# Performance work log

Measured on AMD Instinct MI355X. Metric: run time of the kernel, lower is better.

Reference implementation:

```python
import jax, jax.numpy as jnp
import numpy as np

T, H, I = 8192, 2048, 768  # tokens, hidden_size, intermediate_size

def setup_inputs() -> dict:
    key = jax.random.key(0)
    k1, k2, k3, k4 = jax.random.split(key, 4)
    x = jax.random.normal(k1, (T, H), dtype=jnp.float32)
    # torch nn.Linear weight layout: [out_features, in_features]
    gate_w = jax.random.normal(k2, (I, H), dtype=jnp.float32) * (1.0 / np.sqrt(H))
    up_w = jax.random.normal(k3, (I, H), dtype=jnp.float32) * (1.0 / np.sqrt(H))
    down_w = jax.random.normal(k4, (H, I), dtype=jnp.float32) * (1.0 / np.sqrt(I))
    return {"x": x, "gate_w": gate_w, "up_w": up_w, "down_w": down_w}

def reference(x, gate_w, up_w, down_w):
    # fused SwiGLU MLP: down( silu(x @ gate^T) * (x @ up^T) )
    gate = jnp.einsum('th,ih->ti', x, gate_w)   # [T, I]
    up = jnp.einsum('th,ih->ti', x, up_w)       # [T, I]
    h = jax.nn.silu(gate) * up                   # [T, I]
    out = jnp.einsum('ti,hi->th', h, down_w)     # [T, H]
    return out
```

## Files before the change

kernel.cpp:

```cpp
#include <hip/hip_runtime.h>
#include <hip/hip_bf16.h>
#include <stdint.h>

#define T_DIM 8192
#define H_DIM 2048
#define I_DIM 768

typedef __bf16 bf16_t;
typedef bf16_t bf16x8 __attribute__((ext_vector_type(8)));
typedef bf16_t bf16x4 __attribute__((ext_vector_type(4)));
typedef float  f32x4  __attribute__((ext_vector_type(4)));

__device__ __forceinline__ void async_load16(const void* g, void* s) {
    __builtin_amdgcn_global_load_lds(
        (const __attribute__((address_space(1))) void*)g,
        (__attribute__((address_space(3))) void*)s, 16, 0, 0);
}

__global__ __launch_bounds__(256) void cvt_kernel(
    const float* __restrict__ X, const float* __restrict__ G,
    const float* __restrict__ U, const float* __restrict__ D,
    bf16_t* __restrict__ Xb, bf16_t* __restrict__ Gb,
    bf16_t* __restrict__ Ub, bf16_t* __restrict__ Db)
{
    const size_t N8X = (size_t)T_DIM * H_DIM / 8;
    const size_t N8W = (size_t)I_DIM * H_DIM / 8;
    const size_t total = N8X + 3 * N8W;
    for (size_t i = (size_t)blockIdx.x * blockDim.x + threadIdx.x; i < total;
         i += (size_t)gridDim.x * blockDim.x) {
        const float* s; bf16_t* d; size_t j = i;
        if (j < N8X) { s = X; d = Xb; }
        else {
            j -= N8X;
            if (j < N8W) { s = G; d = Gb; }
            else { j -= N8W;
                if (j < N8W) { s = U; d = Ub; }
                else { j -= N8W; s = D; d = Db; } }
        }
        float4 v0 = ((const float4*)s)[2 * j];
        float4 v1 = ((const float4*)s)[2 * j + 1];
        bf16x8 o;
        o[0] = (bf16_t)v0.x; o[1] = (bf16_t)v0.y; o[2] = (bf16_t)v0.z; o[3] = (bf16_t)v0.w;
        o[4] = (bf16_t)v1.x; o[5] = (bf16_t)v1.y; o[6] = (bf16_t)v1.z; o[7] = (bf16_t)v1.w;
        ((bf16x8*)d)[j] = o;
    }
}


__global__ __launch_bounds__(256) void gateup_kernel(
    const bf16_t* __restrict__ X,
    const bf16_t* __restrict__ Wg,
    const bf16_t* __restrict__ Wu,
    bf16_t* __restrict__ Hbuf)
{
    __shared__ __align__(16) bf16_t sA[128 * 64];
    __shared__ __align__(16) bf16_t sG[64 * 64];
    __shared__ __align__(16) bf16_t sU[64 * 64];

    const int tid   = threadIdx.x;
    const int lane  = tid & 63;
    const int wave  = tid >> 6;
    const int waveM = wave >> 1;
    const int waveN = wave & 1;
    const int quad  = lane >> 4;
    const int lrow  = lane & 15;

    const int blockM = blockIdx.x;
    const int blockN = blockIdx.y;

    f32x4 accG[4][2], accU[4][2];
#pragma unroll
    for (int i = 0; i < 4; i++)
#pragma unroll
        for (int j = 0; j < 2; j++) { accG[i][j] = (f32x4)(0.f); accU[i][j] = (f32x4)(0.f); }

    const bf16_t* Ab = X  + (size_t)(blockM * 128) * H_DIM;
    const bf16_t* Gw = Wg + (size_t)(blockN * 64) * H_DIM;
    const bf16_t* Uw = Wu + (size_t)(blockN * 64) * H_DIM;

    int aRow[4], aCol[4];
#pragma unroll
    for (int i = 0; i < 4; i++) {
        int s = tid + 256 * i;
        aRow[i] = s >> 3;
        aCol[i] = ((s & 7) ^ ((s >> 3) & 7)) * 8;
    }
    int wRow[2], wCol[2];
#pragma unroll
    for (int i = 0; i < 2; i++) {
        int s = tid + 256 * i;
        wRow[i] = s >> 3;
        wCol[i] = ((s & 7) ^ ((s >> 3) & 7)) * 8;
    }

    int aOff[4], wOff[2];
#pragma unroll
    for (int mi = 0; mi < 4; mi++) {
        int r = waveM * 64 + mi * 16 + lrow;
        aOff[mi] = r * 64 + ((quad ^ (r & 7)) * 8);
    }
#pragma unroll
    for (int ni = 0; ni < 2; ni++) {
        int r = waveN * 32 + ni * 16 + lrow;
        wOff[ni] = r * 64 + ((quad ^ (r & 7)) * 8);
    }

    for (int k0 = 0; k0 < H_DIM; k0 += 64) {
#pragma unroll
        for (int i = 0; i < 4; i++)
            async_load16(Ab + (size_t)aRow[i] * H_DIM + k0 + aCol[i],
                         &sA[(tid + 256 * i) * 8]);
#pragma unroll
        for (int i = 0; i < 2; i++) {
            async_load16(Gw + (size_t)wRow[i] * H_DIM + k0 + wCol[i],
                         &sG[(tid + 256 * i) * 8]);
            async_load16(Uw + (size_t)wRow[i] * H_DIM + k0 + wCol[i],
                         &sU[(tid + 256 * i) * 8]);
        }
        __syncthreads();

#pragma unroll
        for (int kk = 0; kk < 2; kk++) {
            const int kx = kk * 32;
            bf16x8 aF[4], gF[2], uF[2];
#pragma unroll
            for (int mi = 0; mi < 4; mi++)
                aF[mi] = *(const bf16x8*)&sA[aOff[mi] ^ kx];
#pragma unroll
            for (int ni = 0; ni < 2; ni++) {
                gF[ni] = *(const bf16x8*)&sG[wOff[ni] ^ kx];
                uF[ni] = *(const bf16x8*)&sU[wOff[ni] ^ kx];
            }
#pragma unroll
            for (int mi = 0; mi < 4; mi++)
#pragma unroll
                for (int ni = 0; ni < 2; ni++) {
                    accG[mi][ni] = __builtin_amdgcn_mfma_f32_16x16x32_bf16(aF[mi], gF[ni], accG[mi][ni], 0, 0, 0);
                    accU[mi][ni] = __builtin_amdgcn_mfma_f32_16x16x32_bf16(aF[mi], uF[ni], accU[mi][ni], 0, 0, 0);
                }
        }
        __syncthreads();
    }

#pragma unroll
    for (int mi = 0; mi < 4; mi++) {
#pragma unroll
        for (int ni = 0; ni < 2; ni++) {
#pragma unroll
            for (int r = 0; r < 4; r++) {
                int row = blockM * 128 + waveM * 64 + mi * 16 + quad * 4 + r;
                int col = blockN * 64 + waveN * 32 + ni * 16 + lrow;
                float g = accG[mi][ni][r];
                float u = accU[mi][ni][r];
                float h = (g / (1.f + __expf(-g))) * u;
                Hbuf[(size_t)row * I_DIM + col] = (bf16_t)h;
            }
        }
    }
}

__global__ __launch_bounds__(256, 4) void down_kernel(
    const bf16_t* __restrict__ Hbuf,
    const bf16_t* __restrict__ Wd,
    float* __restrict__ Out)
{
    __shared__ __align__(16) bf16_t sA[128 * 64];
    __shared__ __align__(16) bf16_t sB[128 * 64];

    const int tid   = threadIdx.x;
    const int lane  = tid & 63;
    const int wave  = tid >> 6;
    const int waveM = wave >> 1;
    const int waveN = wave & 1;
    const int quad  = lane >> 4;
    const int lrow  = lane & 15;

    const int blockM = blockIdx.x;
    const int blockN = blockIdx.y;

    f32x4 acc[4][4];
#pragma unroll
    for (int i = 0; i < 4; i++)
#pragma unroll
        for (int j = 0; j < 4; j++) acc[i][j] = (f32x4)(0.f);

    const bf16_t* Ab = Hbuf + (size_t)(blockM * 128) * I_DIM;
    const bf16_t* Bb = Wd   + (size_t)(blockN * 128) * I_DIM;

    int gRow[4], gCol[4];
#pragma unroll
    for (int i = 0; i < 4; i++) {
        int s = tid + 256 * i;
        gRow[i] = s >> 3;
        gCol[i] = ((s & 7) ^ ((s >> 3) & 7)) * 8;
    }

    int aOff[4], bOff[4];
#pragma unroll
    for (int mi = 0; mi < 4; mi++) {
        int r = waveM * 64 + mi * 16 + lrow;
        aOff[mi] = r * 64 + ((quad ^ (r & 7)) * 8);
    }
#pragma unroll
    for (int ni = 0; ni < 4; ni++) {
        int r = waveN * 64 + ni * 16 + lrow;
        bOff[ni] = r * 64 + ((quad ^ (r & 7)) * 8);
    }

    for (int k0 = 0; k0 < I_DIM; k0 += 64) {
#pragma unroll
        for (int i = 0; i < 4; i++) {
            async_load16(Ab + (size_t)gRow[i] * I_DIM + k0 + gCol[i],
                         &sA[(tid + 256 * i) * 8]);
            async_load16(Bb + (size_t)gRow[i] * I_DIM + k0 + gCol[i],
                         &sB[(tid + 256 * i) * 8]);
        }
        __syncthreads();

#pragma unroll
        for (int kk = 0; kk < 2; kk++) {
            const int kx = kk * 32;
            bf16x8 aF[4], bF[4];
#pragma unroll
            for (int mi = 0; mi < 4; mi++)
                aF[mi] = *(const bf16x8*)&sA[aOff[mi] ^ kx];
#pragma unroll
            for (int ni = 0; ni < 4; ni++)
                bF[ni] = *(const bf16x8*)&sB[bOff[ni] ^ kx];
#pragma unroll
            for (int mi = 0; mi < 4; mi++)
#pragma unroll
                for (int ni = 0; ni < 4; ni++)
                    acc[mi][ni] = __builtin_amdgcn_mfma_f32_16x16x32_bf16(aF[mi], bF[ni], acc[mi][ni], 0, 0, 0);
        }
        __syncthreads();
    }

#pragma unroll
    for (int mi = 0; mi < 4; mi++) {
#pragma unroll
        for (int ni = 0; ni < 4; ni++) {
#pragma unroll
            for (int r = 0; r < 4; r++) {
                int row = blockM * 128 + waveM * 64 + mi * 16 + quad * 4 + r;
                int col = blockN * 128 + waveN * 64 + ni * 16 + lrow;
                Out[(size_t)row * H_DIM + col] = acc[mi][ni][r];
            }
        }
    }
}

extern "C" void kernel_launch(void* const* d_in, const int* in_sizes, int n_in,
                              void* d_out, int out_size, void* d_ws, size_t ws_size,
                              hipStream_t stream) {
    const float* x  = (const float*)d_in[0];
    const float* gw = (const float*)d_in[1];
    const float* uw = (const float*)d_in[2];
    const float* dw = (const float*)d_in[3];
    float* out = (float*)d_out;

    bf16_t* xb = (bf16_t*)d_ws;
    bf16_t* gb = xb + (size_t)T_DIM * H_DIM;
    bf16_t* ub = gb + (size_t)I_DIM * H_DIM;
    bf16_t* db = ub + (size_t)I_DIM * H_DIM;
    bf16_t* hb = db + (size_t)I_DIM * H_DIM;

    cvt_kernel<<<2048, 256, 0, stream>>>(x, gw, uw, dw, xb, gb, ub, db);
    gateup_kernel<<<dim3(T_DIM / 128, I_DIM / 64), 256, 0, stream>>>(xb, gb, ub, hb);
    down_kernel<<<dim3(T_DIM / 128, H_DIM / 128), 256, 0, stream>>>(hb, db, out);
}
```

Before: 238.4 us.

## Shrink gate/up K-tile to 32 and drop LDS swizzle

The gate/up GEMM now stages a K-slice of 32 instead of 64 per iteration, with unswizzled row-major LDS tiles, and loads fragments into registers before a second barrier so the MFMAs run outside the LDS critical section. LDS per block is halved, which could raise occupancy. The cost is twice as many loop iterations and barriers per K, and the plain layout with a 64-byte row stride may bring back LDS bank conflicts on fragment reads.

New measurement: 223.2 us. 1.07x faster.

```diff
diff --git a/kernel.cpp b/kernel.cpp
--- a/kernel.cpp
+++ b/kernel.cpp
@@ -46,16 +46,15 @@
     }
 }
 
-
 __global__ __launch_bounds__(256) void gateup_kernel(
     const bf16_t* __restrict__ X,
     const bf16_t* __restrict__ Wg,
     const bf16_t* __restrict__ Wu,
     bf16_t* __restrict__ Hbuf)
 {
-    __shared__ __align__(16) bf16_t sA[128 * 64];
-    __shared__ __align__(16) bf16_t sG[64 * 64];
-    __shared__ __align__(16) bf16_t sU[64 * 64];
+    __shared__ __align__(16) bf16_t sA[128 * 32];
+    __shared__ __align__(16) bf16_t sG[64 * 32];
+    __shared__ __align__(16) bf16_t sU[64 * 32];
 
     const int tid   = threadIdx.x;
     const int lane  = tid & 63;
@@ -74,72 +73,43 @@
 #pragma unroll
         for (int j = 0; j < 2; j++) { accG[i][j] = (f32x4)(0.f); accU[i][j] = (f32x4)(0.f); }
 
+    const int s0 = tid, s1 = tid + 256;
+    const int rA0 = s0 >> 2, cA0 = (s0 & 3) * 8;
+    const int rA1 = s1 >> 2, cA1 = (s1 & 3) * 8;
+    const int rW  = tid >> 2, cW  = (tid & 3) * 8;
+
     const bf16_t* Ab = X  + (size_t)(blockM * 128) * H_DIM;
-    const bf16_t* Gw = Wg + (size_t)(blockN * 64) * H_DIM;
-    const bf16_t* Uw = Wu + (size_t)(blockN * 64) * H_DIM;
-
-    int aRow[4], aCol[4];
-#pragma unroll
-    for (int i = 0; i < 4; i++) {
-        int s = tid + 256 * i;
-        aRow[i] = s >> 3;
-        aCol[i] = ((s & 7) ^ ((s >> 3) & 7)) * 8;
-    }
-    int wRow[2], wCol[2];
-#pragma unroll
-    for (int i = 0; i < 2; i++) {
-        int s = tid + 256 * i;
-        wRow[i] = s >> 3;
-        wCol[i] = ((s & 7) ^ ((s >> 3) & 7)) * 8;
-    }
-
-    int aOff[4], wOff[2];
-#pragma unroll
-    for (int mi = 0; mi < 4; mi++) {
-        int r = waveM * 64 + mi * 16 + lrow;
-        aOff[mi] = r * 64 + ((quad ^ (r & 7)) * 8);
-    }
-#pragma unroll
-    for (int ni = 0; ni < 2; ni++) {
-        int r = waveN * 32 + ni * 16 + lrow;
-        wOff[ni] = r * 64 + ((quad ^ (r & 7)) * 8);
-    }
-
-    for (int k0 = 0; k0 < H_DIM; k0 += 64) {
-#pragma unroll
-        for (int i = 0; i < 4; i++)
-            async_load16(Ab + (size_t)aRow[i] * H_DIM + k0 + aCol[i],
-                         &sA[(tid + 256 * i) * 8]);
-#pragma unroll
-        for (int i = 0; i < 2; i++) {
-            async_load16(Gw + (size_t)wRow[i] * H_DIM + k0 + wCol[i],
-                         &sG[(tid + 256 * i) * 8]);
-            async_load16(Uw + (size_t)wRow[i] * H_DIM + k0 + wCol[i],
-                         &sU[(tid + 256 * i) * 8]);
-        }
-        __syncthreads();
-
-#pragma unroll
-        for (int kk = 0; kk < 2; kk++) {
-            const int kx = kk * 32;
-            bf16x8 aF[4], gF[2], uF[2];
-#pragma unroll
-            for (int mi = 0; mi < 4; mi++)
-                aF[mi] = *(const bf16x8*)&sA[aOff[mi] ^ kx];
+    const bf16_t* Gb = Wg + (size_t)(blockN * 64) * H_DIM;
+    const bf16_t* Ub = Wu + (size_t)(blockN * 64) * H_DIM;
+
+    for (int k0 = 0; k0 < H_DIM; k0 += 32) {
+        async_load16(Ab + (size_t)rA0 * H_DIM + k0 + cA0, &sA[s0 * 8]);
+        async_load16(Ab + (size_t)rA1 * H_DIM + k0 + cA1, &sA[s1 * 8]);
+        async_load16(Gb + (size_t)rW  * H_DIM + k0 + cW,  &sG[tid * 8]);
+        async_load16(Ub + (size_t)rW  * H_DIM + k0 + cW,  &sU[tid * 8]);
+        __syncthreads();
+
+        bf16x8 aF[4], gF[2], uF[2];
+#pragma unroll
+        for (int mi = 0; mi < 4; mi++) {
+            int r = waveM * 64 + mi * 16 + lrow;
+            aF[mi] = *(const bf16x8*)&sA[r * 32 + quad * 8];
+        }
+#pragma unroll
+        for (int ni = 0; ni < 2; ni++) {
+            int r = waveN * 32 + ni * 16 + lrow;
+            gF[ni] = *(const bf16x8*)&sG[r * 32 + quad * 8];
+            uF[ni] = *(const bf16x8*)&sU[r * 32 + quad * 8];
+        }
+        __syncthreads();
+
+#pragma unroll
+        for (int mi = 0; mi < 4; mi++)
 #pragma unroll
             for (int ni = 0; ni < 2; ni++) {
-                gF[ni] = *(const bf16x8*)&sG[wOff[ni] ^ kx];
-                uF[ni] = *(const bf16x8*)&sU[wOff[ni] ^ kx];
+                accG[mi][ni] = __builtin_amdgcn_mfma_f32_16x16x32_bf16(aF[mi], gF[ni], accG[mi][ni], 0, 0, 0);
+                accU[mi][ni] = __builtin_amdgcn_mfma_f32_16x16x32_bf16(aF[mi], uF[ni], accU[mi][ni], 0, 0, 0);
             }
-#pragma unroll
-            for (int mi = 0; mi < 4; mi++)
-#pragma unroll
-                for (int ni = 0; ni < 2; ni++) {
-                    accG[mi][ni] = __builtin_amdgcn_mfma_f32_16x16x32_bf16(aF[mi], gF[ni], accG[mi][ni], 0, 0, 0);
-                    accU[mi][ni] = __builtin_amdgcn_mfma_f32_16x16x32_bf16(aF[mi], uF[ni], accU[mi][ni], 0, 0, 0);
-                }
-        }
-        __syncthreads();
     }
 
 #pragma unroll
```
